# Kernel optimization log

Measured on AMD Instinct MI355X. Metric: run time of the kernel, lower is better.

## Reference

```python
import jax, jax.numpy as jnp
import numpy as np

N = 20000      # nodes (single node type)
E = 320000     # edges per relation (avg degree 16)
R = 3          # relations / edge types
L = 3          # layers
H = 4          # heads
D = 64         # dim per head (hid_size // n_heads)
IN = 256       # in_size == hid_size
OUT = 128      # out_size
NEG_SLOPE = 0.2


def setup_inputs() -> dict:
    key = jax.random.key(0)
    ks = jax.random.split(key, 8)
    x = jax.random.normal(ks[0], (N, IN), jnp.float32)
    edge_src = jax.random.randint(ks[1], (R, E), 0, N, dtype=jnp.int32)
    edge_dst = jax.random.randint(ks[2], (R, E), 0, N, dtype=jnp.int32)
    W = jax.random.normal(ks[3], (L, R, IN, H * D), jnp.float32) * (1.0 / np.sqrt(IN))
    attn_l = jax.random.normal(ks[4], (L, R, H, D), jnp.float32) * 0.1
    attn_r = jax.random.normal(ks[5], (L, R, H, D), jnp.float32) * 0.1
    bias = jnp.zeros((L, R, H * D), jnp.float32)
    fc_w = jax.random.normal(ks[6], (IN, OUT), jnp.float32) * (1.0 / np.sqrt(IN))
    fc_b = jnp.zeros((OUT,), jnp.float32)
    return dict(x=x, edge_src=edge_src, edge_dst=edge_dst, W=W,
                attn_l=attn_l, attn_r=attn_r, bias=bias, fc_w=fc_w, fc_b=fc_b)


def _gat_conv(h, src, dst, W_r, al, ar, b_r):
    # h: [N, IN] -> feat: [N, H, D]
    feat = (h @ W_r).reshape(N, H, D)
    el = jnp.sum(feat * al, axis=-1)                      # [N, H]
    er = jnp.sum(feat * ar, axis=-1)                      # [N, H]
    e = jax.nn.leaky_relu(el[src] + er[dst], NEG_SLOPE)   # [E, H]
    # segment softmax over incoming edges of each dst node, per head
    m = jax.ops.segment_max(e, dst, num_segments=N)       # [N, H]
    a = jnp.exp(e - m[dst])
    s = jax.ops.segment_sum(a, dst, num_segments=N)       # [N, H]
    alpha = a / s[dst]                                    # [E, H]
    # weighted scatter-add of source features: [N, H, D]
    out = jax.ops.segment_sum(alpha[:, :, None] * feat[src], dst, num_segments=N)
    return out + b_r.reshape(1, H, D)


def reference(x, edge_src, edge_dst, W, attn_l, attn_r, bias, fc_w, fc_b):
    h = x
    for l in range(L):
        acc = jnp.zeros((N, H, D), h.dtype)
        for r in range(R):  # sum-aggregate across relations (HeteroGraphConv aggregate='sum')
            acc = acc + _gat_conv(h, edge_src[r], edge_dst[r],
                                  W[l, r], attn_l[l, r], attn_r[l, r], bias[l, r])
        h = acc.reshape(N, H * D)
        if l != L - 1:
            h = jax.nn.relu(h)  # dropout = identity in eval
    return h @ fc_w + fc_b  # [N, OUT]
```

## Files before the change

### kernel.cpp

```cpp
#include <hip/hip_runtime.h>
#include <math.h>

#define NN 20000
#define NN_PAD 20096
#define EE 320000
#define RR 3
#define LL 3
#define HH 4
#define DD 64
#define CDIM 256
#define OUTD 128
#define NEG 0.2f

typedef float f32x4 __attribute__((ext_vector_type(4)));
typedef short sh8 __attribute__((ext_vector_type(8)));

__device__ __forceinline__ ushort f2bf(float f) {
    union { float f; uint u; } v; v.f = f;
    uint r = (v.u + 0x7FFF + ((v.u >> 16) & 1)) >> 16;
    return (ushort)r;
}
__device__ __forceinline__ float bf2f(ushort u) {
    union { uint u; float f; } v; v.u = ((uint)u) << 16;
    return v.f;
}
__device__ __forceinline__ float bflo(uint p) { return bf2f((ushort)(p & 0xffff)); }
__device__ __forceinline__ float bfhi(uint p) { return bf2f((ushort)(p >> 16)); }

__device__ __forceinline__ void glds16(const ushort* g, ushort* l) {
    __builtin_amdgcn_global_load_lds(
        (const __attribute__((address_space(1))) void*)g,
        (__attribute__((address_space(3))) void*)l, 16, 0, 0);
}


__global__ void count_deg(const int* __restrict__ edge_dst, int* __restrict__ deg) {
    int i = blockIdx.x * blockDim.x + threadIdx.x;
    if (i >= RR * EE) return;
    int r = i / EE;
    atomicAdd(&deg[r * NN + edge_dst[i]], 1);
}

__global__ __launch_bounds__(1024) void scan_kernel(
    const int* __restrict__ deg, int* __restrict__ row_ptr, int* __restrict__ cursor) {
    int r = blockIdx.x;
    const int* d = deg + r * NN;
    int* rp = row_ptr + r * (NN + 1);
    int* cur = cursor + r * (NN + 1);
    __shared__ int wsum[16];
    int lane = threadIdx.x & 63, wv = threadIdx.x >> 6;
    if (threadIdx.x == 0) { rp[0] = 0; cur[0] = 0; }
    int carry = 0;
    for (int base = 0; base < NN; base += 1024) {
        int i = base + threadIdx.x;
        int v = (i < NN) ? d[i] : 0;
        int s = v;
        #pragma unroll
        for (int off = 1; off < 64; off <<= 1) {
            int n = __shfl_up(s, off, 64);
            if (lane >= off) s += n;
        }
        if (lane == 63) wsum[wv] = s;
        __syncthreads();
        if (wv == 0) {
            int ws = (lane < 16) ? wsum[lane] : 0;
            #pragma unroll
            for (int off = 1; off < 16; off <<= 1) {
                int n = __shfl_up(ws, off, 64);
                if (lane >= off) ws += n;
            }
            if (lane < 16) wsum[lane] = ws;
        }
        __syncthreads();
        int incl = carry + (wv ? wsum[wv - 1] : 0) + s;
        if (i < NN) { rp[i + 1] = incl; cur[i + 1] = incl; }
        carry += wsum[15];
        __syncthreads();
    }
}

__global__ void fill_csr(const int* __restrict__ edge_src, const int* __restrict__ edge_dst,
                         int* __restrict__ cursor, int* __restrict__ csr_src) {
    int i = blockIdx.x * blockDim.x + threadIdx.x;
    if (i >= RR * EE) return;
    int r = i / EE;
    int dst = edge_dst[i];
    int pos = atomicAdd(&cursor[r * (NN + 1) + dst], 1);
    csr_src[r * EE + pos] = edge_src[i];
}


__global__ void cvt_bf16x4(const float* __restrict__ in, ushort* __restrict__ out, int n4) {
    int i = blockIdx.x * blockDim.x + threadIdx.x;
    if (i >= n4) return;
    float4 v = *(const float4*)(in + (size_t)i * 4);
    ushort4 o;
    o.x = f2bf(v.x); o.y = f2bf(v.y); o.z = f2bf(v.z); o.w = f2bf(v.w);
    *(ushort4*)(out + (size_t)i * 4) = o;
}

__global__ void prep_all(const float* __restrict__ W, const float* __restrict__ fc_w,
                         ushort* __restrict__ Wt, ushort* __restrict__ fct) {
    __shared__ float tile[32][33];
    int z = blockIdx.z;
    const float* src;
    ushort* dst;
    int N;
    if (z < LL * RR) {
        src = W + (size_t)z * CDIM * CDIM;
        dst = Wt + (size_t)z * CDIM * CDIM;
        N = CDIM;
    } else {
        src = fc_w;
        dst = fct;
        N = OUTD;
    }
    int kb = blockIdx.x * 32, nb = blockIdx.y * 32;
    if (nb >= N) return;
    for (int yy = threadIdx.y; yy < 32; yy += 8)
        tile[yy][threadIdx.x] = src[(size_t)(kb + yy) * N + nb + threadIdx.x];
    __syncthreads();
    for (int yy = threadIdx.y; yy < 32; yy += 8)
        dst[(size_t)(nb + yy) * CDIM + kb + threadIdx.x] = f2bf(tile[threadIdx.x][yy]);
}


#define TM 128
#define TN 128
#define TK 32

__global__ __launch_bounds__(256) void gemm_bf16(
    const ushort* __restrict__ A, const ushort* __restrict__ Bt0, void* __restrict__ C0,
    int M, int K, int Ncol, long strideB, long strideC,
    const float* __restrict__ bias, int out_fp32,
    const float* __restrict__ al_all, const float* __restrict__ ar_all,
    float* __restrict__ el_all, float* __restrict__ er_all) {
    __shared__ alignas(16) ushort As[TM * 32];
    __shared__ alignas(16) ushort Bs[TN * 32];
    const ushort* Bt = Bt0 + (size_t)blockIdx.z * strideB;
    int m0 = blockIdx.x * TM, n0 = blockIdx.y * TN;
    int t = threadIdx.x;
    int wave = t >> 6, lane = t & 63;
    int q = lane >> 4, l16 = lane & 15;
    int wrow = (wave >> 1) * 64, wcol = (wave & 1) * 64;

    int sw = (q ^ ((l16 >> 1) & 3)) * 8;
    int a_off[4], b_off[4];
    #pragma unroll
    for (int i = 0; i < 4; i++) {
        a_off[i] = (wrow + i * 16 + l16) * 32 + sw;
        b_off[i] = (wcol + i * 16 + l16) * 32 + sw;
    }
    int row_a = t >> 2;
    int ch_a  = ((t & 3) ^ ((row_a >> 1) & 3)) * 8;

    f32x4 acc[4][4];
    #pragma unroll
    for (int i = 0; i < 4; i++)
        #pragma unroll
        for (int j = 0; j < 4; j++)
            #pragma unroll
            for (int k = 0; k < 4; k++) acc[i][j][k] = 0.f;

    for (int k0 = 0; k0 < K; k0 += TK) {
        #pragma unroll
        for (int s = 0; s < 2; s++) {
            int qid = t + s * 256;
            int row = row_a + s * 64;
            glds16(A + (size_t)(m0 + row) * K + k0 + ch_a, As + qid * 8);
        }
        #pragma unroll
        for (int s = 0; s < 2; s++) {
            int qid = t + s * 256;
            int row = row_a + s * 64;
            glds16(Bt + (size_t)(n0 + row) * K + k0 + ch_a, Bs + qid * 8);
        }
        __syncthreads();
        sh8 af[4], bfr[4];
        #pragma unroll
        for (int i = 0; i < 4; i++) af[i] = *(const sh8*)(As + a_off[i]);
        #pragma unroll
        for (int j = 0; j < 4; j++) bfr[j] = *(const sh8*)(Bs + b_off[j]);
        #pragma unroll
        for (int i = 0; i < 4; i++)
            #pragma unroll
            for (int j = 0; j < 4; j++)
                acc[i][j] = __builtin_amdgcn_mfma_f32_16x16x32_bf16(af[i], bfr[j], acc[i][j], 0, 0, 0);
        __syncthreads();
    }

    if (out_fp32) {
        float* C = (float*)C0 + (size_t)blockIdx.z * strideC;
        #pragma unroll
        for (int i = 0; i < 4; i++) {
            #pragma unroll
            for (int reg = 0; reg < 4; reg++) {
                int row = m0 + wrow + i * 16 + q * 4 + reg;
                if (row >= M) continue;
                #pragma unroll
                for (int j = 0; j < 4; j++) {
                    int col = n0 + wcol + j * 16 + l16;
                    float v = acc[i][j][reg];
                    if (bias) v += bias[col];
                    C[(size_t)row * Ncol + col] = v;
                }
            }
        }
    } else {
        ushort* C = (ushort*)C0 + (size_t)blockIdx.z * strideC;
        #pragma unroll
        for (int i = 0; i < 4; i++) {
            #pragma unroll
            for (int reg = 0; reg < 4; reg++) {
                int row = m0 + wrow + i * 16 + q * 4 + reg;
                if (row >= M) continue;
                #pragma unroll
                for (int j = 0; j < 4; j++) {
                    int col = n0 + wcol + j * 16 + l16;
                    C[(size_t)row * Ncol + col] = f2bf(acc[i][j][reg]);
                }
            }
        }
    }

    if (el_all) {
        const float* al = al_all + (size_t)blockIdx.z * CDIM;
        const float* ar = ar_all + (size_t)blockIdx.z * CDIM;
        float* elp = el_all + (size_t)blockIdx.z * NN * HH;
        float* erp = er_all + (size_t)blockIdx.z * NN * HH;
        int head = (n0 + wcol) >> 6;
        float alj[4], arj[4];
        #pragma unroll
        for (int j = 0; j < 4; j++) {
            int gcol = n0 + wcol + j * 16 + l16;
            alj[j] = al[gcol];
            arj[j] = ar[gcol];
        }
        #pragma unroll
        for (int i = 0; i < 4; i++) {
            #pragma unroll
            for (int reg = 0; reg < 4; reg++) {
                int row = m0 + wrow + i * 16 + q * 4 + reg;
                float pl = 0.f, pr = 0.f;
                #pragma unroll
                for (int j = 0; j < 4; j++) {
                    pl = fmaf(acc[i][j][reg], alj[j], pl);
                    pr = fmaf(acc[i][j][reg], arj[j], pr);
                }
                #pragma unroll
                for (int m = 1; m < 16; m <<= 1) {
                    pl += __shfl_xor(pl, m, 64);
                    pr += __shfl_xor(pr, m, 64);
                }
                if (l16 == 0 && row < M) {
                    elp[(size_t)row * HH + head] = pl;
                    erp[(size_t)row * HH + head] = pr;
                }
            }
        }
    }
}

__global__ __launch_bounds__(256) void aggregate_fused(
    const ushort* __restrict__ feat16, const float* __restrict__ el,
    const float* __restrict__ er, const int* __restrict__ row_ptr,
    const int* __restrict__ csr_src, const float* __restrict__ bias,
    ushort* __restrict__ hout, int relu) {
    int wv = threadIdx.x >> 6, lane = threadIdx.x & 63;
    int node = blockIdx.x * 4 + wv;
    if (node >= NN) return;
    int c0 = lane * 4;
    int h = lane >> 4;
    float t0 = 0.f, t1 = 0.f, t2 = 0.f, t3 = 0.f;
    #pragma unroll
    for (int r = 0; r < RR; r++) {
        const int* rp = row_ptr + r * (NN + 1);
        int beg = rp[node], end = rp[node + 1];
        const ushort* fr = feat16 + (size_t)r * NN * CDIM;
        const float* elr = el + (size_t)r * NN * HH;
        float ern = er[((size_t)r * NN + node) * HH + h];
        const int* cs = csr_src + (size_t)r * EE;
        float p0 = 0.f, p1 = 0.f, p2 = 0.f, p3 = 0.f, ssum = 0.f;
        int e = beg;
        for (; e + 4 <= end; e += 4) {
            int s0 = cs[e], s1 = cs[e + 1], s2 = cs[e + 2], s3 = cs[e + 3];
            float x0 = elr[s0 * HH + h];
            float x1 = elr[s1 * HH + h];
            float x2 = elr[s2 * HH + h];
            float x3 = elr[s3 * HH + h];
            uint2 f0 = *(const uint2*)(fr + (size_t)s0 * CDIM + c0);
            uint2 f1 = *(const uint2*)(fr + (size_t)s1 * CDIM + c0);
            uint2 f2 = *(const uint2*)(fr + (size_t)s2 * CDIM + c0);
            uint2 f3 = *(const uint2*)(fr + (size_t)s3 * CDIM + c0);
            x0 += ern; x1 += ern; x2 += ern; x3 += ern;
            x0 = x0 > 0.f ? x0 : NEG * x0;
            x1 = x1 > 0.f ? x1 : NEG * x1;
            x2 = x2 > 0.f ? x2 : NEG * x2;
            x3 = x3 > 0.f ? x3 : NEG * x3;
            float a0 = __expf(x0), a1 = __expf(x1), a2 = __expf(x2), a3 = __expf(x3);
            ssum += a0 + a1 + a2 + a3;
            p0 = fmaf(a0, bflo(f0.x), p0); p1 = fmaf(a0, bfhi(f0.x), p1);
            p2 = fmaf(a0, bflo(f0.y), p2); p3 = fmaf(a0, bfhi(f0.y), p3);
            p0 = fmaf(a1, bflo(f1.x), p0); p1 = fmaf(a1, bfhi(f1.x), p1);
            p2 = fmaf(a1, bflo(f1.y), p2); p3 = fmaf(a1, bfhi(f1.y), p3);
            p0 = fmaf(a2, bflo(f2.x), p0); p1 = fmaf(a2, bfhi(f2.x), p1);
            p2 = fmaf(a2, bflo(f2.y), p2); p3 = fmaf(a2, bfhi(f2.y), p3);
            p0 = fmaf(a3, bflo(f3.x), p0); p1 = fmaf(a3, bfhi(f3.x), p1);
            p2 = fmaf(a3, bflo(f3.y), p2); p3 = fmaf(a3, bfhi(f3.y), p3);
        }
        for (; e < end; e++) {
            int s = cs[e];
            float x = elr[s * HH + h] + ern;
            x = x > 0.f ? x : NEG * x;
            float a = __expf(x);
            uint2 f = *(const uint2*)(fr + (size_t)s * CDIM + c0);
            ssum += a;
            p0 = fmaf(a, bflo(f.x), p0); p1 = fmaf(a, bfhi(f.x), p1);
            p2 = fmaf(a, bflo(f.y), p2); p3 = fmaf(a, bfhi(f.y), p3);
        }
        float is = (end > beg) ? 1.f / ssum : 0.f;
        t0 += p0 * is + bias[r * CDIM + c0];
        t1 += p1 * is + bias[r * CDIM + c0 + 1];
        t2 += p2 * is + bias[r * CDIM + c0 + 2];
        t3 += p3 * is + bias[r * CDIM + c0 + 3];
    }
    if (relu) {
        t0 = fmaxf(t0, 0.f); t1 = fmaxf(t1, 0.f);
        t2 = fmaxf(t2, 0.f); t3 = fmaxf(t3, 0.f);
    }
    uint2 o;
    o.x = (uint)f2bf(t0) | ((uint)f2bf(t1) << 16);
    o.y = (uint)f2bf(t2) | ((uint)f2bf(t3) << 16);
    *(uint2*)(hout + (size_t)node * CDIM + c0) = o;
}


extern "C" void kernel_launch(void* const* d_in, const int* in_sizes, int n_in,
                              void* d_out, int out_size, void* d_ws, size_t ws_size,
                              hipStream_t stream) {
    const float* x        = (const float*)d_in[0];
    const int*   edge_src = (const int*)d_in[1];
    const int*   edge_dst = (const int*)d_in[2];
    const float* W        = (const float*)d_in[3];
    const float* attn_l   = (const float*)d_in[4];
    const float* attn_r   = (const float*)d_in[5];
    const float* bias     = (const float*)d_in[6];
    const float* fc_w     = (const float*)d_in[7];
    const float* fc_b     = (const float*)d_in[8];
    float* out = (float*)d_out;

    char* ws = (char*)d_ws;
    size_t off = 0;
    auto alloc = [&](size_t bytes) {
        void* p = ws + off;
        off = (off + bytes + 255) & ~(size_t)255;
        return p;
    };
    ushort* x16    = (ushort*)alloc((size_t)NN_PAD * CDIM * 2);
    ushort* h16    = (ushort*)alloc((size_t)NN_PAD * CDIM * 2);
    ushort* feat16 = (ushort*)alloc((size_t)RR * NN * CDIM * 2);
    ushort* Wt16   = (ushort*)alloc((size_t)LL * RR * CDIM * CDIM * 2);
    ushort* fct16  = (ushort*)alloc((size_t)OUTD * CDIM * 2);
    float* el      = (float*)alloc((size_t)RR * NN * HH * 4);
    float* er      = (float*)alloc((size_t)RR * NN * HH * 4);
    int* row_ptr   = (int*)alloc((size_t)RR * (NN + 1) * 4);
    int* cursor    = (int*)alloc((size_t)RR * (NN + 1) * 4);
    int* csr_src   = (int*)alloc((size_t)RR * EE * 4);
    int* deg       = (int*)alloc((size_t)RR * NN * 4);

    hipMemsetAsync(deg, 0, (size_t)RR * NN * 4, stream);
    count_deg<<<dim3((RR * EE + 255) / 256), dim3(256), 0, stream>>>(edge_dst, deg);
    scan_kernel<<<dim3(RR), dim3(1024), 0, stream>>>(deg, row_ptr, cursor);
    fill_csr<<<dim3((RR * EE + 255) / 256), dim3(256), 0, stream>>>(
        edge_src, edge_dst, cursor, csr_src);

    cvt_bf16x4<<<dim3((NN * CDIM / 4 + 255) / 256), dim3(256), 0, stream>>>(x, x16, NN * CDIM / 4);
    prep_all<<<dim3(CDIM / 32, CDIM / 32, LL * RR + 1), dim3(32, 8), 0, stream>>>(
        W, fc_w, Wt16, fct16);

    const ushort* hin = x16;
    for (int l = 0; l < LL; l++) {
        const ushort* Wl = Wt16 + (size_t)l * RR * CDIM * CDIM;
        dim3 g(NN_PAD / TM, CDIM / TN, RR);
        gemm_bf16<<<g, dim3(256), 0, stream>>>(hin, Wl, feat16, NN, CDIM, CDIM,
                                               (long)CDIM * CDIM, (long)NN * CDIM, nullptr, 0,
                                               attn_l + (size_t)l * RR * CDIM,
                                               attn_r + (size_t)l * RR * CDIM, el, er);
        aggregate_fused<<<dim3(NN / 4), dim3(256), 0, stream>>>(
            feat16, el, er, row_ptr, csr_src, bias + (size_t)l * RR * CDIM,
            h16, (l != LL - 1) ? 1 : 0);
        hin = h16;
    }
    dim3 gf(NN_PAD / TM, OUTD / TN, 1);
    gemm_bf16<<<gf, dim3(256), 0, stream>>>(h16, fct16, out, NN, CDIM, OUTD,
                                            0, 0, fc_b, 1, nullptr, nullptr, nullptr, nullptr);
}
```

Baseline: 515.9 us.

## Split GAT aggregation into alpha precompute and per-head edge-parallel gather

The fused per-node aggregation becomes two kernels. The first computes the unnormalized exp attention weights per edge and head and stores them as bf16 in the no-longer-needed x16 buffer. The second launches one wave per (node, head), with the two half-waves taking alternating edges and a software-pipelined index/weight load, then combines the partial sums by shuffle. The aim is more waves in flight to hide gather latency, at the cost of an extra kernel launch, an extra bf16 write and read of the weights, narrower per-lane loads, and lower precision on the attention weights.

```diff
diff --git a/kernel.cpp b/kernel.cpp
--- a/kernel.cpp
+++ b/kernel.cpp
@@ -261,77 +261,88 @@
     }
 }
 
-__global__ __launch_bounds__(256) void aggregate_fused(
-    const ushort* __restrict__ feat16, const float* __restrict__ el,
-    const float* __restrict__ er, const int* __restrict__ row_ptr,
-    const int* __restrict__ csr_src, const float* __restrict__ bias,
-    ushort* __restrict__ hout, int relu) {
+__global__ __launch_bounds__(256) void attn_alpha(
+    const float* __restrict__ el, const float* __restrict__ er,
+    const int* __restrict__ row_ptr, const int* __restrict__ csr_src,
+    ushort* __restrict__ A) {
     int wv = threadIdx.x >> 6, lane = threadIdx.x & 63;
     int node = blockIdx.x * 4 + wv;
     if (node >= NN) return;
-    int c0 = lane * 4;
-    int h = lane >> 4;
-    float t0 = 0.f, t1 = 0.f, t2 = 0.f, t3 = 0.f;
+    int h = lane >> 4, jj = lane & 15;
     #pragma unroll
     for (int r = 0; r < RR; r++) {
         const int* rp = row_ptr + r * (NN + 1);
         int beg = rp[node], end = rp[node + 1];
-        const ushort* fr = feat16 + (size_t)r * NN * CDIM;
+        const int* cs = csr_src + (size_t)r * EE;
         const float* elr = el + (size_t)r * NN * HH;
         float ern = er[((size_t)r * NN + node) * HH + h];
+        ushort* Ar = A + ((size_t)(r * HH + h)) * EE;
+        for (int e = beg + jj; e < end; e += 16) {
+            int s = cs[e];
+            float x = elr[(size_t)s * HH + h] + ern;
+            x = x > 0.f ? x : NEG * x;
+            Ar[e] = f2bf(__expf(x));
+        }
+    }
+}
+
+__global__ __launch_bounds__(256) void agg_pass2(
+    const ushort* __restrict__ feat16, const ushort* __restrict__ A,
+    const int* __restrict__ row_ptr, const int* __restrict__ csr_src,
+    const float* __restrict__ bias, ushort* __restrict__ hout, int relu) {
+    int bid = blockIdx.x;
+    int chunk = (bid & 7) >> 1;
+    int par = bid & 1;
+    int grp = bid >> 3;
+    int wv = threadIdx.x >> 6, lane = threadIdx.x & 63;
+    int node = grp * 8 + par * 4 + wv;
+    if (node >= NN) return;
+    int h = chunk;
+    int j = lane >> 5, c = lane & 31;
+    int ch = h * 64 + 2 * c;
+
+    float t0 = 0.f, t1 = 0.f;
+    #pragma unroll
+    for (int r = 0; r < RR; r++) {
+        const int* rp = row_ptr + r * (NN + 1);
+        int beg = rp[node], end = rp[node + 1];
         const int* cs = csr_src + (size_t)r * EE;
-        float p0 = 0.f, p1 = 0.f, p2 = 0.f, p3 = 0.f, ssum = 0.f;
-        int e = beg;
-        for (; e + 4 <= end; e += 4) {
-            int s0 = cs[e], s1 = cs[e + 1], s2 = cs[e + 2], s3 = cs[e + 3];
-            float x0 = elr[s0 * HH + h];
-            float x1 = elr[s1 * HH + h];
-            float x2 = elr[s2 * HH + h];
-            float x3 = elr[s3 * HH + h];
-            uint2 f0 = *(const uint2*)(fr + (size_t)s0 * CDIM + c0);
-            uint2 f1 = *(const uint2*)(fr + (size_t)s1 * CDIM + c0);
-            uint2 f2 = *(const uint2*)(fr + (size_t)s2 * CDIM + c0);
-            uint2 f3 = *(const uint2*)(fr + (size_t)s3 * CDIM + c0);
-            x0 += ern; x1 += ern; x2 += ern; x3 += ern;
-            x0 = x0 > 0.f ? x0 : NEG * x0;
-            x1 = x1 > 0.f ? x1 : NEG * x1;
-            x2 = x2 > 0.f ? x2 : NEG * x2;
-            x3 = x3 > 0.f ? x3 : NEG * x3;
-            float a0 = __expf(x0), a1 = __expf(x1), a2 = __expf(x2), a3 = __expf(x3);
-            ssum += a0 + a1 + a2 + a3;
-            p0 = fmaf(a0, bflo(f0.x), p0); p1 = fmaf(a0, bfhi(f0.x), p1);
-            p2 = fmaf(a0, bflo(f0.y), p2); p3 = fmaf(a0, bfhi(f0.y), p3);
-            p0 = fmaf(a1, bflo(f1.x), p0); p1 = fmaf(a1, bfhi(f1.x), p1);
-            p2 = fmaf(a1, bflo(f1.y), p2); p3 = fmaf(a1, bfhi(f1.y), p3);
-            p0 = fmaf(a2, bflo(f2.x), p0); p1 = fmaf(a2, bfhi(f2.x), p1);
-            p2 = fmaf(a2, bflo(f2.y), p2); p3 = fmaf(a2, bfhi(f2.y), p3);
-            p0 = fmaf(a3, bflo(f3.x), p0); p1 = fmaf(a3, bfhi(f3.x), p1);
-            p2 = fmaf(a3, bflo(f3.y), p2); p3 = fmaf(a3, bfhi(f3.y), p3);
-        }
-        for (; e < end; e++) {
+        const ushort* Ar = A + ((size_t)(r * HH + h)) * EE;
+        const ushort* fr = feat16 + (size_t)r * NN * CDIM;
+        float p0 = 0.f, p1 = 0.f, ss = 0.f;
+        int e = beg + j;
+        if (e < end) {
             int s = cs[e];
-            float x = elr[s * HH + h] + ern;
-            x = x > 0.f ? x : NEG * x;
-            float a = __expf(x);
-            uint2 f = *(const uint2*)(fr + (size_t)s * CDIM + c0);
-            ssum += a;
-            p0 = fmaf(a, bflo(f.x), p0); p1 = fmaf(a, bfhi(f.x), p1);
-            p2 = fmaf(a, bflo(f.y), p2); p3 = fmaf(a, bfhi(f.y), p3);
-        }
-        float is = (end > beg) ? 1.f / ssum : 0.f;
-        t0 += p0 * is + bias[r * CDIM + c0];
-        t1 += p1 * is + bias[r * CDIM + c0 + 1];
-        t2 += p2 * is + bias[r * CDIM + c0 + 2];
-        t3 += p3 * is + bias[r * CDIM + c0 + 3];
-    }
-    if (relu) {
-        t0 = fmaxf(t0, 0.f); t1 = fmaxf(t1, 0.f);
-        t2 = fmaxf(t2, 0.f); t3 = fmaxf(t3, 0.f);
-    }
-    uint2 o;
-    o.x = (uint)f2bf(t0) | ((uint)f2bf(t1) << 16);
-    o.y = (uint)f2bf(t2) | ((uint)f2bf(t3) << 16);
-    *(uint2*)(hout + (size_t)node * CDIM + c0) = o;
+            float a = bf2f(Ar[e]);
+            for (e += 2; e < end; e += 2) {
+                int sn = cs[e];
+                float an = bf2f(Ar[e]);
+                uint f = *(const uint*)(fr + (size_t)s * CDIM + ch);
+                ss += a;
+                p0 = fmaf(a, bflo(f), p0);
+                p1 = fmaf(a, bfhi(f), p1);
+                s = sn; a = an;
+            }
+            uint f = *(const uint*)(fr + (size_t)s * CDIM + ch);
+            ss += a;
+            p0 = fmaf(a, bflo(f), p0);
+            p1 = fmaf(a, bfhi(f), p1);
+        }
+        ss += __shfl_xor(ss, 32, 64);
+        float is = (end > beg) ? 1.f / ss : 0.f;
+        t0 = fmaf(p0, is, t0);
+        t1 = fmaf(p1, is, t1);
+        float2 b = *(const float2*)(bias + r * CDIM + ch);
+        t0 += 0.5f * b.x;
+        t1 += 0.5f * b.y;
+    }
+    t0 += __shfl_xor(t0, 32, 64);
+    t1 += __shfl_xor(t1, 32, 64);
+    if (relu) { t0 = fmaxf(t0, 0.f); t1 = fmaxf(t1, 0.f); }
+    if (j == 0) {
+        uint o = (uint)f2bf(t0) | ((uint)f2bf(t1) << 16);
+        *(uint*)(hout + (size_t)node * CDIM + ch) = o;
+    }
 }
 
 
@@ -367,6 +378,7 @@
     int* cursor    = (int*)alloc((size_t)RR * (NN + 1) * 4);
     int* csr_src   = (int*)alloc((size_t)RR * EE * 4);
     int* deg       = (int*)alloc((size_t)RR * NN * 4);
+    ushort* Aw = x16;
 
     hipMemsetAsync(deg, 0, (size_t)RR * NN * 4, stream);
     count_deg<<<dim3((RR * EE + 255) / 256), dim3(256), 0, stream>>>(edge_dst, deg);
@@ -386,8 +398,9 @@
                                                (long)CDIM * CDIM, (long)NN * CDIM, nullptr, 0,
                                                attn_l + (size_t)l * RR * CDIM,
                                                attn_r + (size_t)l * RR * CDIM, el, er);
-        aggregate_fused<<<dim3(NN / 4), dim3(256), 0, stream>>>(
-            feat16, el, er, row_ptr, csr_src, bias + (size_t)l * RR * CDIM,
+        attn_alpha<<<dim3(NN / 4), dim3(256), 0, stream>>>(el, er, row_ptr, csr_src, Aw);
+        agg_pass2<<<dim3(NN), dim3(256), 0, stream>>>(
+            feat16, Aw, row_ptr, csr_src, bias + (size_t)l * RR * CDIM,
             h16, (l != LL - 1) ? 1 : 0);
         hin = h16;
     }
```

Result: slower. 718.2 us (+39.2%).
